# Kernel optimization log

Hardware: AMD Instinct MI355X
Metric: run time of the kernel (lower is better)

## Reference

```python
import jax, jax.numpy as jnp
import numpy as np
from jax import lax

N, T = 1024, 128
A_DIM, Z_DIM, H_DIM = 8, 32, 256


def setup_inputs() -> dict:
    key = jax.random.key(0)
    ks = jax.random.split(key, 12)
    s = 0.1  # small init scale for numerical stability of the recurrence
    return {
        "A": jax.random.normal(ks[0], (N, T, A_DIM), jnp.float32),
        "eps": jax.random.normal(ks[1], (N, T, Z_DIM), jnp.float32),
        "z0": jnp.zeros((1, Z_DIM), jnp.float32),
        "h0": jnp.zeros((1, H_DIM), jnp.float32),
        "c0": jnp.zeros((1, H_DIM), jnp.float32),
        "W_ih": jax.random.normal(ks[2], (4 * H_DIM, A_DIM + Z_DIM), jnp.float32) * s,
        "W_hh": jax.random.normal(ks[3], (4 * H_DIM, H_DIM), jnp.float32) * s,
        "b_ih": jax.random.normal(ks[4], (4 * H_DIM,), jnp.float32) * s,
        "b_hh": jax.random.normal(ks[5], (4 * H_DIM,), jnp.float32) * s,
        "W1": jax.random.normal(ks[6], (128, H_DIM), jnp.float32) * s,
        "b1": jax.random.normal(ks[7], (128,), jnp.float32) * s,
        "W2": jax.random.normal(ks[8], (128, 128), jnp.float32) * s,
        "b2": jax.random.normal(ks[9], (128,), jnp.float32) * s,
        "Wz": jax.random.normal(ks[10], (2 * Z_DIM, 128), jnp.float32) * s,
        "bz": jax.random.normal(ks[11], (2 * Z_DIM,), jnp.float32) * s,
    }


def reference(A, eps, z0, h0, c0, W_ih, W_hh, b_ih, b_hh, W1, b1, W2, b2, Wz, bz):
    """BayesianSequenceModel.guide: per-step LSTMCell + encoder MLP +
    reparameterized Gaussian draw z_t = loc + softplus(raw_scale) * eps_t.
    Returns Z with shape [N, T, z_size]."""
    n = A.shape[0]
    zdim = eps.shape[-1]

    def step(carry, xs):
        z, h, c = carry
        a_t, e_t = xs
        x = jnp.concatenate([a_t, z], axis=-1)                    # [N, a+z]
        gates = x @ W_ih.T + b_ih + h @ W_hh.T + b_hh             # [N, 4H]
        i, f, g, o = jnp.split(gates, 4, axis=-1)                 # torch LSTMCell order
        c_new = jax.nn.sigmoid(f) * c + jax.nn.sigmoid(i) * jnp.tanh(g)
        h_new = jax.nn.sigmoid(o) * jnp.tanh(c_new)
        # Encoder
        u = jax.nn.relu(h_new @ W1.T + b1)
        u = jax.nn.relu(u @ W2.T + b2)
        zz = u @ Wz.T + bz                                        # [N, 2*zdim]
        z_loc = zz[:, :zdim]
        z_scale = jax.nn.softplus(zz[:, zdim:])
        z_new = z_loc + z_scale * e_t                             # reparameterized sample
        return (z_new, h_new, c_new), z_new

    carry0 = (
        jnp.broadcast_to(z0, (n, z0.shape[1])),
        jnp.broadcast_to(h0, (n, h0.shape[1])),
        jnp.broadcast_to(c0, (n, c0.shape[1])),
    )
    xs = (jnp.swapaxes(A, 0, 1), jnp.swapaxes(eps, 0, 1))         # time-major
    _, Zs = lax.scan(step, carry0, xs)                            # [T, N, zdim]
    return jnp.swapaxes(Zs, 0, 1)                                 # [N, T, zdim]
```

## Files before the change

### kernel.cpp

```cpp
#include <hip/hip_runtime.h>
#include <hip/hip_bf16.h>
#include <math.h>

typedef __bf16 bf16x8 __attribute__((ext_vector_type(8)));
typedef float floatx4 __attribute__((ext_vector_type(4)));

#define T_LEN 128

#define WP_OFF   0
#define WP_SZ    (64*10*64*16)
#define W1P_OFF  (WP_OFF + WP_SZ)
#define W1P_SZ   (8*8*64*16)
#define W2P_OFF  (W1P_OFF + W1P_SZ)
#define W2P_SZ   (8*4*64*16)
#define WZP_OFF  (W2P_OFF + W2P_SZ)
#define WZP_SZ   (4*4*64*16)
#define WS_NEEDED ((size_t)(WZP_OFF + WZP_SZ))

#define WAITVM(N) (((N) & 0xF) | (0x7 << 4) | (0xF << 8) | (((N) >> 4) << 14))

#define BAR() do {                                                  \
    asm volatile("s_waitcnt lgkmcnt(0)" ::: "memory");              \
    __builtin_amdgcn_sched_barrier(0);                              \
    __builtin_amdgcn_s_barrier();                                   \
    __builtin_amdgcn_sched_barrier(0);                              \
} while (0)

#if __has_builtin(__builtin_amdgcn_exp2f)
#define EXP2F(x) __builtin_amdgcn_exp2f(x)
#else
#define EXP2F(x) exp2f(x)
#endif
#if __has_builtin(__builtin_amdgcn_logf)
#define LOG2F(x) __builtin_amdgcn_logf(x)
#else
#define LOG2F(x) log2f(x)
#endif
#if __has_builtin(__builtin_amdgcn_rcpf)
#define RCPF(x) __builtin_amdgcn_rcpf(x)
#else
#define RCPF(x) (1.0f/(x))
#endif

__device__ __forceinline__ float fsigmoid(float x) {
    return RCPF(1.0f + EXP2F(-1.4426950408889634f * x));
}
__device__ __forceinline__ float ftanh(float x) {
    return 1.0f - 2.0f * RCPF(1.0f + EXP2F(2.8853900817779268f * x));
}

__device__ __forceinline__ void dma16(const void* g, void* lds) {
    __builtin_amdgcn_global_load_lds(
        (const __attribute__((address_space(1))) void*)g,
        (__attribute__((address_space(3))) void*)lds,
        16, 0, 0);
}

__global__ void prep_kernel(const float* __restrict__ Wih, const float* __restrict__ Whh,
                            const float* __restrict__ W1,  const float* __restrict__ W2,
                            const float* __restrict__ Wz,  unsigned char* __restrict__ ws)
{
    int id = blockIdx.x * blockDim.x + threadIdx.x;
    __bf16* Wp  = (__bf16*)(ws + WP_OFF);
    __bf16* W1p = (__bf16*)(ws + W1P_OFF);
    __bf16* W2p = (__bf16*)(ws + W2P_OFF);
    __bf16* Wzp = (__bf16*)(ws + WZP_OFF);
    if (id < 40960) {
        int ct = id / 640, rem = id % 640;
        int ki = rem / 64, lane = rem % 64;
        int row = ct * 16 + (lane & 15);
        int kb  = ki * 32 + (lane >> 4) * 8;
        for (int j = 0; j < 8; ++j) {
            int k = kb + j;
            float v;
            if (k < 40)       v = Wih[row * 40 + k];
            else if (k < 296) v = Whh[row * 256 + (k - 40)];
            else              v = 0.0f;
            Wp[((size_t)(ki * 64 + ct) * 64 + lane) * 8 + j] = (__bf16)v;
        }
    } else if (id < 45056) {
        int id2 = id - 40960;
        int rem = id2 % 512, lane = rem % 64;
        int row = (id2 / 512) * 16 + (lane & 15);
        int kb  = (rem / 64) * 32 + (lane >> 4) * 8;
        for (int j = 0; j < 8; ++j) W1p[(size_t)id2 * 8 + j] = (__bf16)W1[row * 256 + kb + j];
    } else if (id < 47104) {
        int id3 = id - 45056;
        int rem = id3 % 256, lane = rem % 64;
        int row = (id3 / 256) * 16 + (lane & 15);
        int kb  = (rem / 64) * 32 + (lane >> 4) * 8;
        for (int j = 0; j < 8; ++j) W2p[(size_t)id3 * 8 + j] = (__bf16)W2[row * 128 + kb + j];
    } else if (id < 48128) {
        int id4 = id - 47104;
        int rem = id4 % 256, lane = rem % 64;
        int row = (id4 / 256) * 16 + (lane & 15);
        int kb  = (rem / 64) * 32 + (lane >> 4) * 8;
        for (int j = 0; j < 8; ++j) Wzp[(size_t)id4 * 8 + j] = (__bf16)Wz[row * 128 + kb + j];
    }
}

__global__ __launch_bounds__(512) void seq_mfma(
    const float* __restrict__ A,   const float* __restrict__ eps,
    const float* __restrict__ z0,  const float* __restrict__ h0,
    const float* __restrict__ c0,
    const float* __restrict__ bih, const float* __restrict__ bhh,
    const float* __restrict__ b1,  const float* __restrict__ b2,
    const float* __restrict__ bz,
    const unsigned char* __restrict__ ws, float* __restrict__ out)
{
    const int tid  = threadIdx.x;
    const int w    = tid >> 6;
    const int lane = tid & 63;
    const int lrow = lane & 15;
    const int quad = lane >> 4;
    const int n0   = blockIdx.x * 16;

    __shared__ __align__(16) __bf16 slots[8][2][2048];
    __shared__ __align__(16) __bf16 wmlp2[(W2P_SZ + WZP_SZ) / 2];
    __shared__ __align__(16) __bf16 xh[2][16][328];
    __shared__ __align__(16) __bf16 u1s[16][136];
    __shared__ __align__(16) __bf16 u2s[16][136];
    float* zzf = (float*)&u1s[0][0];

    const char* wsb = (const char*)ws;

    {
        const float4* src = (const float4*)(wsb + W2P_OFF);
        float4* dst = (float4*)wmlp2;
        for (int i = tid; i < 3072; i += 512) dst[i] = src[i];
    }
    const __bf16* w2l = wmlp2;
    const __bf16* wzl = wmlp2 + 16384;

    for (int idx = tid; idx < 2 * 16 * 320; idx += 512) {
        int b = idx / (16 * 320);
        int rem = idx % (16 * 320);
        int r = rem / 320, col = rem % 320;
        float v;
        if (col >= 8 && col < 40)        v = z0[col - 8];
        else if (col >= 40 && col < 296) v = h0[col - 40];
        else                             v = 0.0f;
        xh[b][r][col] = (__bf16)v;
    }
    if (tid < 128)
        xh[0][tid >> 3][tid & 7] =
            (__bf16)A[((size_t)(n0 + (tid >> 3)) * T_LEN + 0) * 8 + (tid & 7)];

    bf16x8 w1f[8];
    #pragma unroll
    for (int k = 0; k < 8; ++k)
        w1f[k] = *(const bf16x8*)(wsb + W1P_OFF + ((size_t)(w * 8 + k) * 64 + lane) * 16);

    float gb[4][2];
    #pragma unroll
    for (int g = 0; g < 4; ++g)
        #pragma unroll
        for (int j = 0; j < 2; ++j) {
            int unit = 32 * w + 16 * j + lrow;
            gb[g][j] = bih[g * 256 + unit] + bhh[g * 256 + unit];
        }
    float u1b = b1[w * 16 + lrow];
    float u2b = b2[w * 16 + lrow];
    float zzb = (w < 4) ? bz[w * 16 + lrow] : 0.0f;
    float cst[2][4];
    #pragma unroll
    for (int j = 0; j < 2; ++j) {
        float cv = c0[32 * w + 16 * j + lrow];
        #pragma unroll
        for (int r = 0; r < 4; ++r) cst[j][r] = cv;
    }

    #define ISSUEK0(H) do {                                                     \
        _Pragma("unroll")                                                       \
        for (int gg = 0; gg < 2; ++gg)                                          \
            _Pragma("unroll")                                                   \
            for (int j = 0; j < 2; ++j)                                         \
                dma16(wsb + WP_OFF +                                            \
                      ((size_t)((2 * (H) + gg) * 16 + 2 * w + j) * 1024) +      \
                      (size_t)lane * 16,                                        \
                      (void*)&slots[w][H][(gg * 2 + j) * 512]);                 \
    } while (0)

    ISSUEK0(0);
    ISSUEK0(1);
    __syncthreads();

    #define GHALF(KI, H, NW, DOREF) do {                                        \
        __builtin_amdgcn_s_waitcnt(WAITVM(NW));                                 \
        __builtin_amdgcn_sched_barrier(0);                                      \
        _Pragma("unroll")                                                       \
        for (int gg = 0; gg < 2; ++gg)                                          \
            _Pragma("unroll")                                                   \
            for (int j = 0; j < 2; ++j) {                                       \
                bf16x8 b_ = *(const bf16x8*)&slots[w][H][(gg * 2 + j) * 512 +   \
                                                         lane * 8];             \
                acc[2 * (H) + gg][j] = __builtin_amdgcn_mfma_f32_16x16x32_bf16( \
                    af, b_, acc[2 * (H) + gg][j], 0, 0, 0);                     \
            }                                                                   \
        __builtin_amdgcn_sched_barrier(0);                                      \
        if (DOREF) {                                                            \
            _Pragma("unroll")                                                   \
            for (int gg = 0; gg < 2; ++gg)                                      \
                _Pragma("unroll")                                               \
                for (int j = 0; j < 2; ++j)                                     \
                    dma16(wsb + WP_OFF + (size_t)((KI) + 1) * 65536 +           \
                          ((size_t)((2 * (H) + gg) * 16 + 2 * w + j) * 1024) +  \
                          (size_t)lane * 16,                                    \
                          (void*)&slots[w][H][(gg * 2 + j) * 512]);             \
        }                                                                       \
    } while (0)

    #define GKI(KI, NA, NB, DOREF) do {                                         \
        bf16x8 af = *(const bf16x8*)&xh[cb][lrow][(KI) * 32 + quad * 8];        \
        GHALF(KI, 0, NA, DOREF);                                                \
        GHALF(KI, 1, NB, DOREF);                                                \
    } while (0)

    for (int t = 0; t < T_LEN; ++t) {
        const int cb = t & 1;
        const int nb = cb ^ 1;

        float eps_cur = eps[((size_t)(n0 + (tid >> 5)) * T_LEN + t) * 32 + (tid & 31)];
        float a_nxt = 0.0f;
        if (t + 1 < T_LEN && tid < 128)
            a_nxt = A[((size_t)(n0 + (tid >> 3)) * T_LEN + (t + 1)) * 8 + (tid & 7)];

        floatx4 acc[4][2];
        #pragma unroll
        for (int g = 0; g < 4; ++g)
            #pragma unroll
            for (int j = 0; j < 2; ++j)
                acc[g][j] = (floatx4){gb[g][j], gb[g][j], gb[g][j], gb[g][j]};

        GKI(0, 7, 7, 1);
        GKI(1, 4, 4, 1);
        GKI(2, 4, 4, 1);
        GKI(3, 4, 4, 1);
        GKI(4, 4, 4, 1);
        GKI(5, 4, 4, 1);
        GKI(6, 4, 4, 1);
        GKI(7, 4, 4, 1);
        GKI(8, 4, 4, 1);
        GKI(9, 4, 0, 0);

        #pragma unroll
        for (int j = 0; j < 2; ++j)
            #pragma unroll
            for (int r = 0; r < 4; ++r) {
                float iv = fsigmoid(acc[0][j][r]);
                float fv = fsigmoid(acc[1][j][r]);
                float gv = ftanh(acc[2][j][r]);
                float ov = fsigmoid(acc[3][j][r]);
                float cn = fv * cst[j][r] + iv * gv;
                cst[j][r] = cn;
                xh[nb][quad * 4 + r][40 + 32 * w + 16 * j + lrow] = (__bf16)(ov * ftanh(cn));
            }
        if (t + 1 < T_LEN && tid < 128)
            xh[nb][tid >> 3][tid & 7] = (__bf16)a_nxt;
        BAR();

        {
            floatx4 a1 = (floatx4){u1b, u1b, u1b, u1b};
            #pragma unroll
            for (int ki = 0; ki < 8; ++ki) {
                bf16x8 af = *(const bf16x8*)&xh[nb][lrow][40 + ki * 32 + quad * 8];
                a1 = __builtin_amdgcn_mfma_f32_16x16x32_bf16(af, w1f[ki], a1, 0, 0, 0);
            }
            #pragma unroll
            for (int r = 0; r < 4; ++r)
                u1s[quad * 4 + r][w * 16 + lrow] = (__bf16)fmaxf(a1[r], 0.0f);
        }
        BAR();

        {
            floatx4 a2 = (floatx4){u2b, u2b, u2b, u2b};
            #pragma unroll
            for (int ki = 0; ki < 4; ++ki) {
                bf16x8 af = *(const bf16x8*)&u1s[lrow][ki * 32 + quad * 8];
                bf16x8 bb = *(const bf16x8*)&w2l[w * 2048 + ki * 512 + lane * 8];
                a2 = __builtin_amdgcn_mfma_f32_16x16x32_bf16(af, bb, a2, 0, 0, 0);
            }
            #pragma unroll
            for (int r = 0; r < 4; ++r)
                u2s[quad * 4 + r][w * 16 + lrow] = (__bf16)fmaxf(a2[r], 0.0f);
        }
        ISSUEK0(0);
        BAR();

        if (w < 4) {
            floatx4 a3 = (floatx4){zzb, zzb, zzb, zzb};
            #pragma unroll
            for (int ki = 0; ki < 4; ++ki) {
                bf16x8 af = *(const bf16x8*)&u2s[lrow][ki * 32 + quad * 8];
                bf16x8 bb = *(const bf16x8*)&wzl[w * 2048 + ki * 512 + lane * 8];
                a3 = __builtin_amdgcn_mfma_f32_16x16x32_bf16(af, bb, a3, 0, 0, 0);
            }
            #pragma unroll
            for (int r = 0; r < 4; ++r)
                zzf[(quad * 4 + r) * 68 + w * 16 + lrow] = a3[r];
        }
        ISSUEK0(1);
        BAR();

        {
            int r = tid >> 5, c = tid & 31;
            float loc = zzf[r * 68 + c];
            float raw = zzf[r * 68 + c + 32];
            float sp  = (raw > 20.0f)
                      ? raw
                      : 0.6931471805599453f *
                        LOG2F(1.0f + EXP2F(1.4426950408889634f * raw));
            float zv  = loc + sp * eps_cur;
            xh[nb][r][8 + c] = (__bf16)zv;
            out[((size_t)(n0 + r) * T_LEN + t) * 32 + c] = zv;
        }
        BAR();
    }
    #undef GKI
    #undef GHALF
    #undef ISSUEK0
}

struct SM {
    float zx[4][40]; float h[4][256]; float u1[4][128]; float u2[4][128]; float zz[4][64];
};

__global__ __launch_bounds__(256) void seq_valu(
    const float* __restrict__ A, const float* __restrict__ eps,
    const float* __restrict__ z0, const float* __restrict__ h0, const float* __restrict__ c0,
    const float* __restrict__ Wih, const float* __restrict__ Whh,
    const float* __restrict__ bih, const float* __restrict__ bhh,
    const float* __restrict__ W1, const float* __restrict__ b1,
    const float* __restrict__ W2, const float* __restrict__ b2,
    const float* __restrict__ Wz, const float* __restrict__ bz, float* __restrict__ out)
{
    __shared__ SM sm;
    const int tid = threadIdx.x;
    const int n0  = blockIdx.x * 4;
    if (tid < 128) { int rr = tid >> 5, cc = tid & 31; sm.zx[rr][8 + cc] = z0[cc]; }
    for (int i = tid; i < 4 * 256; i += 256) sm.h[i >> 8][i & 255] = h0[i & 255];
    float c[4];
    #pragma unroll
    for (int rr = 0; rr < 4; ++rr) c[rr] = c0[tid];
    float gbias[4];
    #pragma unroll
    for (int g = 0; g < 4; ++g) gbias[g] = bih[g * 256 + tid] + bhh[g * 256 + tid];

    for (int t = 0; t < T_LEN; ++t) {
        if (tid < 32) { int rr = tid >> 3, cc = tid & 7;
            sm.zx[rr][cc] = A[((size_t)(n0 + rr) * T_LEN + t) * 8 + cc]; }
        __syncthreads();
        float acc[4][4];
        #pragma unroll
        for (int g = 0; g < 4; ++g)
            #pragma unroll
            for (int rr = 0; rr < 4; ++rr) acc[g][rr] = gbias[g];
        for (int k = 0; k < 40; ++k) {
            float xv[4];
            #pragma unroll
            for (int rr = 0; rr < 4; ++rr) xv[rr] = sm.zx[rr][k];
            #pragma unroll
            for (int g = 0; g < 4; ++g) {
                float w = Wih[(size_t)(g * 256 + tid) * 40 + k];
                #pragma unroll
                for (int rr = 0; rr < 4; ++rr) acc[g][rr] += w * xv[rr];
            }
        }
        for (int k = 0; k < 256; ++k) {
            float hv[4];
            #pragma unroll
            for (int rr = 0; rr < 4; ++rr) hv[rr] = sm.h[rr][k];
            #pragma unroll
            for (int g = 0; g < 4; ++g) {
                float w = Whh[(size_t)(g * 256 + tid) * 256 + k];
                #pragma unroll
                for (int rr = 0; rr < 4; ++rr) acc[g][rr] += w * hv[rr];
            }
        }
        __syncthreads();
        #pragma unroll
        for (int rr = 0; rr < 4; ++rr) {
            float iv = 1.0f / (1.0f + expf(-acc[0][rr]));
            float fv = 1.0f / (1.0f + expf(-acc[1][rr]));
            float gv = tanhf(acc[2][rr]);
            float ov = 1.0f / (1.0f + expf(-acc[3][rr]));
            float cn = fv * c[rr] + iv * gv;
            c[rr] = cn;
            sm.h[rr][tid] = ov * tanhf(cn);
        }
        __syncthreads();
        { int col = tid & 127, rb = (tid >> 7) * 2;
          float a0 = b1[col], a1 = a0;
          for (int k = 0; k < 256; ++k) { float w = W1[(size_t)col * 256 + k];
              a0 += w * sm.h[rb][k]; a1 += w * sm.h[rb + 1][k]; }
          sm.u1[rb][col] = fmaxf(a0, 0.0f); sm.u1[rb + 1][col] = fmaxf(a1, 0.0f); }
        __syncthreads();
        { int col = tid & 127, rb = (tid >> 7) * 2;
          float a0 = b2[col], a1 = a0;
          for (int k = 0; k < 128; ++k) { float w = W2[(size_t)col * 128 + k];
              a0 += w * sm.u1[rb][k]; a1 += w * sm.u1[rb + 1][k]; }
          sm.u2[rb][col] = fmaxf(a0, 0.0f); sm.u2[rb + 1][col] = fmaxf(a1, 0.0f); }
        __syncthreads();
        { int rr = tid >> 6, col = tid & 63;
// ... 49 lines not shown
```

Before: 1.340 ms.

## Software-pipeline encoder MLP into next step's LSTM gate GEMM

Reorders the packed K dimension so h comes first, then z, then a. The encoder's first layer (h @ W1) can then be computed alongside the h-part of the next step's gate GEMM, and the z-dependent and a-dependent K chunks are deferred until after the encoder output is ready. The z output projection and softplus sampling are fused into two waves writing directly to xh and out, which removes the zz staging buffer and one barrier. The last timestep's encoder is peeled into an epilogue. The intent is to shorten the per-step serial critical path, at the cost of more complex weight-streaming order and wait counts.

```diff
diff --git a/kernel.cpp b/kernel.cpp
--- a/kernel.cpp
+++ b/kernel.cpp
@@ -73,8 +73,9 @@
         for (int j = 0; j < 8; ++j) {
             int k = kb + j;
             float v;
-            if (k < 40)       v = Wih[row * 40 + k];
-            else if (k < 296) v = Whh[row * 256 + (k - 40)];
+            if (k < 256)      v = Whh[row * 256 + k];
+            else if (k < 288) v = Wih[row * 40 + 8 + (k - 256)];
+            else if (k < 296) v = Wih[row * 40 + (k - 288)];
             else              v = 0.0f;
             Wp[((size_t)(ki * 64 + ct) * 64 + lane) * 8 + j] = (__bf16)v;
         }
@@ -120,7 +121,6 @@
     __shared__ __align__(16) __bf16 xh[2][16][328];
     __shared__ __align__(16) __bf16 u1s[16][136];
     __shared__ __align__(16) __bf16 u2s[16][136];
-    float* zzf = (float*)&u1s[0][0];
 
     const char* wsb = (const char*)ws;
 
@@ -137,13 +137,13 @@
         int rem = idx % (16 * 320);
         int r = rem / 320, col = rem % 320;
         float v;
-        if (col >= 8 && col < 40)        v = z0[col - 8];
-        else if (col >= 40 && col < 296) v = h0[col - 40];
-        else                             v = 0.0f;
+        if (col < 256)      v = h0[col];
+        else if (col < 288) v = z0[col - 256];
+        else                v = 0.0f;
         xh[b][r][col] = (__bf16)v;
     }
     if (tid < 128)
-        xh[0][tid >> 3][tid & 7] =
+        xh[0][tid >> 3][288 + (tid & 7)] =
             (__bf16)A[((size_t)(n0 + (tid >> 3)) * T_LEN + 0) * 8 + (tid & 7)];
 
     bf16x8 w1f[8];
@@ -161,7 +161,8 @@
         }
     float u1b = b1[w * 16 + lrow];
     float u2b = b2[w * 16 + lrow];
-    float zzb = (w < 4) ? bz[w * 16 + lrow] : 0.0f;
+    float bzl = bz[(w & 1) * 16 + lrow];
+    float bzr = bz[32 + (w & 1) * 16 + lrow];
     float cst[2][4];
     #pragma unroll
     for (int j = 0; j < 2; ++j) {
@@ -170,79 +171,128 @@
         for (int r = 0; r < 4; ++r) cst[j][r] = cv;
     }
 
-    #define ISSUEK0(H) do {                                                     \
+    #define WAITN(N) do { __builtin_amdgcn_s_waitcnt(WAITVM(N)); \
+        __builtin_amdgcn_sched_barrier(0); } while (0)
+    #define RFILL(RKI, H) do {                                                  \
         _Pragma("unroll")                                                       \
         for (int gg = 0; gg < 2; ++gg)                                          \
             _Pragma("unroll")                                                   \
             for (int j = 0; j < 2; ++j)                                         \
-                dma16(wsb + WP_OFF +                                            \
+                dma16(wsb + WP_OFF + (size_t)(RKI) * 65536 +                    \
                       ((size_t)((2 * (H) + gg) * 16 + 2 * w + j) * 1024) +      \
                       (size_t)lane * 16,                                        \
                       (void*)&slots[w][H][(gg * 2 + j) * 512]);                 \
     } while (0)
-
-    ISSUEK0(0);
-    ISSUEK0(1);
-    __syncthreads();
-
-    #define GHALF(KI, H, NW, DOREF) do {                                        \
-        __builtin_amdgcn_s_waitcnt(WAITVM(NW));                                 \
-        __builtin_amdgcn_sched_barrier(0);                                      \
+    #define CHALF(H) do {                                                       \
         _Pragma("unroll")                                                       \
         for (int gg = 0; gg < 2; ++gg)                                          \
             _Pragma("unroll")                                                   \
             for (int j = 0; j < 2; ++j) {                                       \
-                bf16x8 b_ = *(const bf16x8*)&slots[w][H][(gg * 2 + j) * 512 +   \
-                                                         lane * 8];             \
+                bf16x8 b_ = *(const bf16x8*)&slots[w][H][(gg * 2 + j) * 512     \
+                                                         + lane * 8];           \
                 acc[2 * (H) + gg][j] = __builtin_amdgcn_mfma_f32_16x16x32_bf16( \
                     af, b_, acc[2 * (H) + gg][j], 0, 0, 0);                     \
             }                                                                   \
         __builtin_amdgcn_sched_barrier(0);                                      \
-        if (DOREF) {                                                            \
-            _Pragma("unroll")                                                   \
-            for (int gg = 0; gg < 2; ++gg)                                      \
-                _Pragma("unroll")                                               \
-                for (int j = 0; j < 2; ++j)                                     \
-                    dma16(wsb + WP_OFF + (size_t)((KI) + 1) * 65536 +           \
-                          ((size_t)((2 * (H) + gg) * 16 + 2 * w + j) * 1024) +  \
-                          (size_t)lane * 16,                                    \
-                          (void*)&slots[w][H][(gg * 2 + j) * 512]);             \
-        }                                                                       \
     } while (0)
-
-    #define GKI(KI, NA, NB, DOREF) do {                                         \
+    #define GATEKI(KI, RKI, WA, WB) do {                                        \
         bf16x8 af = *(const bf16x8*)&xh[cb][lrow][(KI) * 32 + quad * 8];        \
-        GHALF(KI, 0, NA, DOREF);                                                \
-        GHALF(KI, 1, NB, DOREF);                                                \
+        WAITN(WA); CHALF(0); RFILL(RKI, 0);                                     \
+        WAITN(WB); CHALF(1); RFILL(RKI, 1);                                     \
     } while (0)
+    #define GATEKI_U1(KI, RKI, WA, WB) do {                                     \
+        bf16x8 af = *(const bf16x8*)&xh[cb][lrow][(KI) * 32 + quad * 8];        \
+        WAITN(WA); CHALF(0); RFILL(RKI, 0);                                     \
+        WAITN(WB); CHALF(1); RFILL(RKI, 1);                                     \
+        a1 = __builtin_amdgcn_mfma_f32_16x16x32_bf16(af, w1f[KI], a1, 0, 0, 0); \
+    } while (0)
+
+    RFILL(0, 0);
+    RFILL(0, 1);
+    __syncthreads();
+
+    float epsr[4];
+    float av = 0.0f;
+    const int aidx = (w & 1) * 64 + lane;
 
     for (int t = 0; t < T_LEN; ++t) {
         const int cb = t & 1;
         const int nb = cb ^ 1;
 
-        float eps_cur = eps[((size_t)(n0 + (tid >> 5)) * T_LEN + t) * 32 + (tid & 31)];
-        float a_nxt = 0.0f;
-        if (t + 1 < T_LEN && tid < 128)
-            a_nxt = A[((size_t)(n0 + (tid >> 3)) * T_LEN + (t + 1)) * 8 + (tid & 7)];
-
         floatx4 acc[4][2];
         #pragma unroll
         for (int g = 0; g < 4; ++g)
             #pragma unroll
             for (int j = 0; j < 2; ++j)
                 acc[g][j] = (floatx4){gb[g][j], gb[g][j], gb[g][j], gb[g][j]};
-
-        GKI(0, 7, 7, 1);
-        GKI(1, 4, 4, 1);
-        GKI(2, 4, 4, 1);
-        GKI(3, 4, 4, 1);
-        GKI(4, 4, 4, 1);
-        GKI(5, 4, 4, 1);
-        GKI(6, 4, 4, 1);
-        GKI(7, 4, 4, 1);
-        GKI(8, 4, 4, 1);
-        GKI(9, 4, 0, 0);
-
+        floatx4 a1 = (floatx4){u1b, u1b, u1b, u1b};
+
+        GATEKI_U1(0, 1, 4, 4);
+        __builtin_amdgcn_sched_barrier(0);
+        {
+            const int te = (t > 0) ? (t - 1) : 0;
+            #pragma unroll
+            for (int r = 0; r < 4; ++r)
+                epsr[r] = eps[((size_t)(n0 + quad * 4 + r) * T_LEN + te) * 32
+                              + (w & 1) * 16 + lrow];
+            const int ta = (t + 1 < T_LEN) ? (t + 1) : (T_LEN - 1);
+            av = A[((size_t)(n0 + (aidx >> 3)) * T_LEN + ta) * 8 + (aidx & 7)];
+        }
+        __builtin_amdgcn_sched_barrier(0);
+        GATEKI_U1(1, 2, 9, 9);
+        GATEKI_U1(2, 3, 4, 4);
+        GATEKI_U1(3, 4, 4, 4);
+        GATEKI_U1(4, 5, 4, 4);
+        GATEKI_U1(5, 6, 4, 4);
+        GATEKI_U1(6, 7, 4, 4);
+        GATEKI_U1(7, 9, 4, 4);
+        #pragma unroll
+        for (int r = 0; r < 4; ++r)
+            u1s[quad * 4 + r][w * 16 + lrow] = (__bf16)fmaxf(a1[r], 0.0f);
+        BAR();
+
+        GATEKI(9, 8, 4, 4);
+        {
+            floatx4 a2 = (floatx4){u2b, u2b, u2b, u2b};
+            #pragma unroll
+            for (int ki = 0; ki < 4; ++ki) {
+                bf16x8 af = *(const bf16x8*)&u1s[lrow][ki * 32 + quad * 8];
+                bf16x8 bb = *(const bf16x8*)&w2l[w * 2048 + ki * 512 + lane * 8];
+                a2 = __builtin_amdgcn_mfma_f32_16x16x32_bf16(af, bb, a2, 0, 0, 0);
+            }
+            #pragma unroll
+            for (int r = 0; r < 4; ++r)
+                u2s[quad * 4 + r][w * 16 + lrow] = (__bf16)fmaxf(a2[r], 0.0f);
+        }
+        BAR();
+
+        if (w < 2 && t > 0) {
+            floatx4 aL = (floatx4){bzl, bzl, bzl, bzl};
+            floatx4 aR = (floatx4){bzr, bzr, bzr, bzr};
+            #pragma unroll
+            for (int ki = 0; ki < 4; ++ki) {
+                bf16x8 af = *(const bf16x8*)&u2s[lrow][ki * 32 + quad * 8];
+                bf16x8 bl = *(const bf16x8*)&wzl[(w)     * 2048 + ki * 512 + lane * 8];
+                bf16x8 br = *(const bf16x8*)&wzl[(w + 2) * 2048 + ki * 512 + lane * 8];
+                aL = __builtin_amdgcn_mfma_f32_16x16x32_bf16(af, bl, aL, 0, 0, 0);
+                aR = __builtin_amdgcn_mfma_f32_16x16x32_bf16(af, br, aR, 0, 0, 0);
+            }
+            #pragma unroll
+            for (int r = 0; r < 4; ++r) {
+                float raw = aR[r];
+                float sp  = (raw > 20.0f)
+                          ? raw
+                          : 0.6931471805599453f *
+                            LOG2F(1.0f + EXP2F(1.4426950408889634f * raw));
+                float zv  = aL[r] + sp * epsr[r];
+                xh[cb][quad * 4 + r][256 + w * 16 + lrow] = (__bf16)zv;
+                out[((size_t)(n0 + quad * 4 + r) * T_LEN + (t - 1)) * 32
+                    + w * 16 + lrow] = zv;
+            }
+        }
+        BAR();
+
+        GATEKI(8, 0, 4, 4);
         #pragma unroll
         for (int j = 0; j < 2; ++j)
             #pragma unroll
@@ -253,72 +303,70 @@
                 float ov = fsigmoid(acc[3][j][r]);
                 float cn = fv * cst[j][r] + iv * gv;
                 cst[j][r] = cn;
-                xh[nb][quad * 4 + r][40 + 32 * w + 16 * j + lrow] = (__bf16)(ov * ftanh(cn));
-            }
-        if (t + 1 < T_LEN && tid < 128)
-            xh[nb][tid >> 3][tid & 7] = (__bf16)a_nxt;
+                xh[nb][quad * 4 + r][32 * w + 16 * j + lrow] = (__bf16)(ov * ftanh(cn));
+            }
+        if (w < 2 && t + 1 < T_LEN)
+            xh[nb][aidx >> 3][288 + (aidx & 7)] = (__bf16)av;
         BAR();
-
-        {
-            floatx4 a1 = (floatx4){u1b, u1b, u1b, u1b};
-            #pragma unroll
-            for (int ki = 0; ki < 8; ++ki) {
-                bf16x8 af = *(const bf16x8*)&xh[nb][lrow][40 + ki * 32 + quad * 8];
-                a1 = __builtin_amdgcn_mfma_f32_16x16x32_bf16(af, w1f[ki], a1, 0, 0, 0);
-            }
-            #pragma unroll
-            for (int r = 0; r < 4; ++r)
-                u1s[quad * 4 + r][w * 16 + lrow] = (__bf16)fmaxf(a1[r], 0.0f);
-        }
+    }
+
+    asm volatile("s_waitcnt vmcnt(0)" ::: "memory");
+    __builtin_amdgcn_sched_barrier(0);
+    {
+        #pragma unroll
+        for (int r = 0; r < 4; ++r)
+            epsr[r] = eps[((size_t)(n0 + quad * 4 + r) * T_LEN + (T_LEN - 1)) * 32
+                          + (w & 1) * 16 + lrow];
+        floatx4 a1 = (floatx4){u1b, u1b, u1b, u1b};
+        #pragma unroll
+        for (int ki = 0; ki < 8; ++ki) {
+            bf16x8 af = *(const bf16x8*)&xh[0][lrow][ki * 32 + quad * 8];
+            a1 = __builtin_amdgcn_mfma_f32_16x16x32_bf16(af, w1f[ki], a1, 0, 0, 0);
+        }
+        #pragma unroll
+        for (int r = 0; r < 4; ++r)
+            u1s[quad * 4 + r][w * 16 + lrow] = (__bf16)fmaxf(a1[r], 0.0f);
         BAR();
-
-        {
-            floatx4 a2 = (floatx4){u2b, u2b, u2b, u2b};
-            #pragma unroll
-            for (int ki = 0; ki < 4; ++ki) {
-                bf16x8 af = *(const bf16x8*)&u1s[lrow][ki * 32 + quad * 8];
-                bf16x8 bb = *(const bf16x8*)&w2l[w * 2048 + ki * 512 + lane * 8];
-                a2 = __builtin_amdgcn_mfma_f32_16x16x32_bf16(af, bb, a2, 0, 0, 0);
-            }
-            #pragma unroll
-            for (int r = 0; r < 4; ++r)
-                u2s[quad * 4 + r][w * 16 + lrow] = (__bf16)fmaxf(a2[r], 0.0f);
-        }
-        ISSUEK0(0);
+        floatx4 a2 = (floatx4){u2b, u2b, u2b, u2b};
+        #pragma unroll
+        for (int ki = 0; ki < 4; ++ki) {
+            bf16x8 af = *(const bf16x8*)&u1s[lrow][ki * 32 + quad * 8];
+            bf16x8 bb = *(const bf16x8*)&w2l[w * 2048 + ki * 512 + lane * 8];
+            a2 = __builtin_amdgcn_mfma_f32_16x16x32_bf16(af, bb, a2, 0, 0, 0);
+        }
+        #pragma unroll
+        for (int r = 0; r < 4; ++r)
+            u2s[quad * 4 + r][w * 16 + lrow] = (__bf16)fmaxf(a2[r], 0.0f);
         BAR();
-
-        if (w < 4) {
-            floatx4 a3 = (floatx4){zzb, zzb, zzb, zzb};
+        if (w < 2) {
+            floatx4 aL = (floatx4){bzl, bzl, bzl, bzl};
+            floatx4 aR = (floatx4){bzr, bzr, bzr, bzr};
             #pragma unroll
             for (int ki = 0; ki < 4; ++ki) {
                 bf16x8 af = *(const bf16x8*)&u2s[lrow][ki * 32 + quad * 8];
-                bf16x8 bb = *(const bf16x8*)&wzl[w * 2048 + ki * 512 + lane * 8];
-                a3 = __builtin_amdgcn_mfma_f32_16x16x32_bf16(af, bb, a3, 0, 0, 0);
-            }
-            #pragma unroll
-            for (int r = 0; r < 4; ++r)
-                zzf[(quad * 4 + r) * 68 + w * 16 + lrow] = a3[r];
-        }
-        ISSUEK0(1);
-        BAR();
-
-        {
-            int r = tid >> 5, c = tid & 31;
-            float loc = zzf[r * 68 + c];
-            float raw = zzf[r * 68 + c + 32];
-            float sp  = (raw > 20.0f)
-                      ? raw
-                      : 0.6931471805599453f *
-                        LOG2F(1.0f + EXP2F(1.4426950408889634f * raw));
-            float zv  = loc + sp * eps_cur;
-            xh[nb][r][8 + c] = (__bf16)zv;
-            out[((size_t)(n0 + r) * T_LEN + t) * 32 + c] = zv;
-        }
-        BAR();
-    }
-    #undef GKI
-    #undef GHALF
-    #undef ISSUEK0
+                bf16x8 bl = *(const bf16x8*)&wzl[(w)     * 2048 + ki * 512 + lane * 8];
+                bf16x8 br = *(const bf16x8*)&wzl[(w + 2) * 2048 + ki * 512 + lane * 8];
+                aL = __builtin_amdgcn_mfma_f32_16x16x32_bf16(af, bl, aL, 0, 0, 0);
+                aR = __builtin_amdgcn_mfma_f32_16x16x32_bf16(af, br, aR, 0, 0, 0);
+            }
+            #pragma unroll
+            for (int r = 0; r < 4; ++r) {
+                float raw = aR[r];
+                float sp  = (raw > 20.0f)
+                          ? raw
+                          : 0.6931471805599453f *
+                            LOG2F(1.0f + EXP2F(1.4426950408889634f * raw));
+                float zv  = aL[r] + sp * epsr[r];
+                out[((size_t)(n0 + quad * 4 + r) * T_LEN + (T_LEN - 1)) * 32
+                    + w * 16 + lrow] = zv;
+            }
+        }
+    }
+    #undef GATEKI_U1
+    #undef GATEKI
+    #undef CHALF
+    #undef RFILL
+    #undef WAITN
 }
 
 struct SM {
```

Result: slower. 1.599 ms (+19.3%).

## Deepen weight-streaming pipeline to four slots and stream MLP weights through it

Applied to the files above, without the earlier changes.

Replaces the two-slot per-wave gate weight ring with a four-slot ring, prefetching two k-chunks ahead so DMA has more time to land before each MFMA consumes it. The W2 and Wz MLP weights are no longer held resident in LDS; they are streamed through the same ring each step, which frees LDS. The time loop is unrolled by two so slot indices become compile-time constants, and the eps/A loads for the next step are issued early. The cost is extra global/L2 traffic for the MLP weights every step and more vmcnt bookkeeping that must stay exactly right.

```diff
diff --git a/kernel.cpp b/kernel.cpp
--- a/kernel.cpp
+++ b/kernel.cpp
@@ -115,22 +115,13 @@
     const int quad = lane >> 4;
     const int n0   = blockIdx.x * 16;
 
-    __shared__ __align__(16) __bf16 slots[8][2][2048];
-    __shared__ __align__(16) __bf16 wmlp2[(W2P_SZ + WZP_SZ) / 2];
+    __shared__ __align__(16) __bf16 slots[8][4][2048];
     __shared__ __align__(16) __bf16 xh[2][16][328];
     __shared__ __align__(16) __bf16 u1s[16][136];
     __shared__ __align__(16) __bf16 u2s[16][136];
     float* zzf = (float*)&u1s[0][0];
 
     const char* wsb = (const char*)ws;
-
-    {
-        const float4* src = (const float4*)(wsb + W2P_OFF);
-        float4* dst = (float4*)wmlp2;
-        for (int i = tid; i < 3072; i += 512) dst[i] = src[i];
-    }
-    const __bf16* w2l = wmlp2;
-    const __bf16* wzl = wmlp2 + 16384;
 
     for (int idx = tid; idx < 2 * 16 * 320; idx += 512) {
         int b = idx / (16 * 320);
@@ -170,155 +161,198 @@
         for (int r = 0; r < 4; ++r) cst[j][r] = cv;
     }
 
-    #define ISSUEK0(H) do {                                                     \
+    #define DMAG(KI, H, SL) do {                                                \
         _Pragma("unroll")                                                       \
         for (int gg = 0; gg < 2; ++gg)                                          \
             _Pragma("unroll")                                                   \
             for (int j = 0; j < 2; ++j)                                         \
-                dma16(wsb + WP_OFF +                                            \
+                dma16(wsb + WP_OFF + (size_t)(KI) * 65536 +                     \
                       ((size_t)((2 * (H) + gg) * 16 + 2 * w + j) * 1024) +      \
                       (size_t)lane * 16,                                        \
-                      (void*)&slots[w][H][(gg * 2 + j) * 512]);                 \
+                      (void*)&slots[w][SL][(gg * 2 + j) * 512]);                \
     } while (0)
-
-    ISSUEK0(0);
-    ISSUEK0(1);
-    __syncthreads();
-
-    #define GHALF(KI, H, NW, DOREF) do {                                        \
-        __builtin_amdgcn_s_waitcnt(WAITVM(NW));                                 \
+    #define DMAW2(SL) do {                                                      \
+        _Pragma("unroll")                                                       \
+        for (int i = 0; i < 4; ++i)                                             \
+            dma16(wsb + W2P_OFF + (size_t)w * 4096 + i * 1024 +                 \
+                  (size_t)lane * 16, (void*)&slots[w][SL][i * 512]);            \
+    } while (0)
+    #define DMAWZ(SL) do {                                                      \
+        _Pragma("unroll")                                                       \
+        for (int i = 0; i < 4; ++i)                                             \
+            dma16(wsb + WZP_OFF + (size_t)(w & 3) * 4096 + i * 1024 +           \
+                  (size_t)lane * 16, (void*)&slots[w][SL][i * 512]);            \
+    } while (0)
+    #define CONSG(H, SL, WN) do {                                               \
+        __builtin_amdgcn_s_waitcnt(WAITVM(WN));                                 \
         __builtin_amdgcn_sched_barrier(0);                                      \
         _Pragma("unroll")                                                       \
         for (int gg = 0; gg < 2; ++gg)                                          \
             _Pragma("unroll")                                                   \
             for (int j = 0; j < 2; ++j) {                                       \
-                bf16x8 b_ = *(const bf16x8*)&slots[w][H][(gg * 2 + j) * 512 +   \
-                                                         lane * 8];             \
+                bf16x8 b_ = *(const bf16x8*)&slots[w][SL][(gg * 2 + j) * 512    \
+                                                          + lane * 8];          \
                 acc[2 * (H) + gg][j] = __builtin_amdgcn_mfma_f32_16x16x32_bf16( \
                     af, b_, acc[2 * (H) + gg][j], 0, 0, 0);                     \
             }                                                                   \
         __builtin_amdgcn_sched_barrier(0);                                      \
-        if (DOREF) {                                                            \
-            _Pragma("unroll")                                                   \
-            for (int gg = 0; gg < 2; ++gg)                                      \
+    } while (0)
+
+    const int aidx = (w & 1) * 64 + lane;
+    float eps_cur, eps_nxt, av;
+
+    DMAG(0, 0, 0);
+    DMAG(0, 1, 1);
+    DMAG(1, 0, 2);
+    DMAG(1, 1, 3);
+    eps_cur = eps[((size_t)(n0 + (tid >> 5)) * T_LEN + 0) * 32 + (tid & 31)];
+    av      = A[((size_t)(n0 + (aidx >> 3)) * T_LEN + 1) * 8 + (aidx & 7)];
+    __syncthreads();
+
+    #define STEPBODY(OFF, T) do {                                               \
+        const int cb = (T) & 1;                                                 \
+        const int nb = cb ^ 1;                                                  \
+        floatx4 acc[4][2];                                                      \
+        _Pragma("unroll")                                                       \
+        for (int g = 0; g < 4; ++g)                                             \
+            _Pragma("unroll")                                                   \
+            for (int j = 0; j < 2; ++j)                                         \
+                acc[g][j] = (floatx4){gb[g][j], gb[g][j], gb[g][j], gb[g][j]};  \
+        {               \
+            bf16x8 af;                                                          \
+            af = *(const bf16x8*)&xh[cb][lrow][0 * 32 + quad * 8];              \
+            CONSG(0, (0  + (OFF)) & 3, 14);  DMAG(2, 0, (0  + (OFF)) & 3);      \
+            CONSG(1, (1  + (OFF)) & 3, 14);  DMAG(2, 1, (1  + (OFF)) & 3);      \
+            af = *(const bf16x8*)&xh[cb][lrow][1 * 32 + quad * 8];              \
+            CONSG(0, (2  + (OFF)) & 3, 14);  DMAG(3, 0, (2  + (OFF)) & 3);      \
+            CONSG(1, (3  + (OFF)) & 3, 14);  DMAG(3, 1, (3  + (OFF)) & 3);      \
+            af = *(const bf16x8*)&xh[cb][lrow][2 * 32 + quad * 8];              \
+            CONSG(0, (4  + (OFF)) & 3, 12);  DMAG(4, 0, (4  + (OFF)) & 3);      \
+            CONSG(1, (5  + (OFF)) & 3, 12);  DMAG(4, 1, (5  + (OFF)) & 3);      \
+            af = *(const bf16x8*)&xh[cb][lrow][3 * 32 + quad * 8];              \
+            CONSG(0, (6  + (OFF)) & 3, 12);  DMAG(5, 0, (6  + (OFF)) & 3);      \
+            CONSG(1, (7  + (OFF)) & 3, 12);  DMAG(5, 1, (7  + (OFF)) & 3);      \
+            af = *(const bf16x8*)&xh[cb][lrow][4 * 32 + quad * 8];              \
+            CONSG(0, (8  + (OFF)) & 3, 12);  DMAG(6, 0, (8  + (OFF)) & 3);      \
+            CONSG(1, (9  + (OFF)) & 3, 12);  DMAG(6, 1, (9  + (OFF)) & 3);      \
+            af = *(const bf16x8*)&xh[cb][lrow][5 * 32 + quad * 8];              \
+            CONSG(0, (10 + (OFF)) & 3, 12);  DMAG(7, 0, (10 + (OFF)) & 3);      \
+            CONSG(1, (11 + (OFF)) & 3, 12);  DMAG(7, 1, (11 + (OFF)) & 3);      \
+            af = *(const bf16x8*)&xh[cb][lrow][6 * 32 + quad * 8];              \
+            CONSG(0, (12 + (OFF)) & 3, 12);  DMAG(8, 0, (12 + (OFF)) & 3);      \
+            CONSG(1, (13 + (OFF)) & 3, 12);  DMAG(8, 1, (13 + (OFF)) & 3);      \
+            af = *(const bf16x8*)&xh[cb][lrow][7 * 32 + quad * 8];              \
+            CONSG(0, (14 + (OFF)) & 3, 12);  DMAG(9, 0, (14 + (OFF)) & 3);      \
+            CONSG(1, (15 + (OFF)) & 3, 12);  DMAG(9, 1, (15 + (OFF)) & 3);      \
+            af = *(const bf16x8*)&xh[cb][lrow][8 * 32 + quad * 8];              \
+            CONSG(0, (16 + (OFF)) & 3, 12);  DMAW2((16 + (OFF)) & 3);           \
+            CONSG(1, (17 + (OFF)) & 3, 12);  DMAWZ((17 + (OFF)) & 3);           \
+            af = *(const bf16x8*)&xh[cb][lrow][9 * 32 + quad * 8];              \
+            CONSG(0, (18 + (OFF)) & 3, 12);  DMAG(0, 0, (18 + (OFF)) & 3);      \
+            CONSG(1, (19 + (OFF)) & 3, 12);  DMAG(0, 1, (19 + (OFF)) & 3);      \
+        }                                                                       \
+                       \
+        _Pragma("unroll")                                                       \
+        for (int j = 0; j < 2; ++j)                                             \
+            _Pragma("unroll")                                                   \
+            for (int r = 0; r < 4; ++r) {                                       \
+                float iv = fsigmoid(acc[0][j][r]);                              \
+                float fv = fsigmoid(acc[1][j][r]);                              \
+                float gv = ftanh(acc[2][j][r]);                                 \
+                float ov = fsigmoid(acc[3][j][r]);                              \
+                float cn = fv * cst[j][r] + iv * gv;                            \
+                cst[j][r] = cn;                                                 \
+                xh[nb][quad * 4 + r][40 + 32 * w + 16 * j + lrow] =             \
+                    (__bf16)(ov * ftanh(cn));                                   \
+            }                                                                   \
+        if (w < 2 && (T) + 1 < T_LEN)                                           \
+            xh[nb][aidx >> 3][aidx & 7] = (__bf16)av;                           \
+        BAR();                                    \
+        {                       \
+            floatx4 a1 = (floatx4){u1b, u1b, u1b, u1b};                         \
+            _Pragma("unroll")                                                   \
+            for (int ki = 0; ki < 8; ++ki) {                                    \
+                bf16x8 af1 = *(const bf16x8*)&xh[nb][lrow][40 + ki * 32         \
+                                                           + quad * 8];        \
+                a1 = __builtin_amdgcn_mfma_f32_16x16x32_bf16(af1, w1f[ki],      \
+                                                             a1, 0, 0, 0);      \
+            }                                                                   \
+            _Pragma("unroll")                                                   \
+            for (int r = 0; r < 4; ++r)                                         \
+                u1s[quad * 4 + r][w * 16 + lrow] = (__bf16)fmaxf(a1[r], 0.0f);  \
+        }                                                                       \
+        BAR();                                               \
+        {                 \
+            __builtin_amdgcn_s_waitcnt(WAITVM(12));                             \
+            __builtin_amdgcn_sched_barrier(0);                                  \
+            floatx4 a2 = (floatx4){u2b, u2b, u2b, u2b};                         \
+            _Pragma("unroll")                                                   \
+            for (int ki = 0; ki < 4; ++ki) {                                    \
+                bf16x8 af2 = *(const bf16x8*)&u1s[lrow][ki * 32 + quad * 8];    \
+                bf16x8 bb  = *(const bf16x8*)&slots[w][(20 + (OFF)) & 3]        \
+                                                      [ki * 512 + lane * 8];    \
+                a2 = __builtin_amdgcn_mfma_f32_16x16x32_bf16(af2, bb,           \
+                                                             a2, 0, 0, 0);      \
+            }                                                                   \
+            _Pragma("unroll")                                                   \
+            for (int r = 0; r < 4; ++r)                                         \
+                u2s[quad * 4 + r][w * 16 + lrow] = (__bf16)fmaxf(a2[r], 0.0f);  \
+            __builtin_amdgcn_sched_barrier(0);                                  \
+            DMAG(1, 0, (20 + (OFF)) & 3);                                       \
+        }                                                                       \
+        BAR();                     \
+        {        \
+            __builtin_amdgcn_s_waitcnt(WAITVM(12));                             \
+            __builtin_amdgcn_sched_barrier(0);                                  \
+            if (w < 4) {                                                        \
+                floatx4 a3 = (floatx4){zzb, zzb, zzb, zzb};                     \
                 _Pragma("unroll")                                               \
-                for (int j = 0; j < 2; ++j)                                     \
-                    dma16(wsb + WP_OFF + (size_t)((KI) + 1) * 65536 +           \
-                          ((size_t)((2 * (H) + gg) * 16 + 2 * w + j) * 1024) +  \
-                          (size_t)lane * 16,                                    \
-                          (void*)&slots[w][H][(gg * 2 + j) * 512]);             \
+                for (int ki = 0; ki < 4; ++ki) {                                \
+                    bf16x8 af3 = *(const bf16x8*)&u2s[lrow][ki * 32             \
+                                                            + quad * 8];       \
+                    bf16x8 bb  = *(const bf16x8*)&slots[w][(21 + (OFF)) & 3]    \
+                                                          [ki * 512 + lane * 8];\
+                    a3 = __builtin_amdgcn_mfma_f32_16x16x32_bf16(af3, bb,       \
+                                                                 a3, 0, 0, 0);  \
+                }                                                               \
+                _Pragma("unroll")                                               \
+                for (int r = 0; r < 4; ++r)                                     \
+                    zzf[(quad * 4 + r) * 68 + w * 16 + lrow] = a3[r];           \
+            }                                                                   \
+            __builtin_amdgcn_sched_barrier(0);                                  \
+            DMAG(1, 1, (21 + (OFF)) & 3);                                       \
+            const int te = ((T) + 1 < T_LEN) ? (T) + 1 : T_LEN - 1;             \
+            eps_nxt = eps[((size_t)(n0 + (tid >> 5)) * T_LEN + te) * 32         \
+                          + (tid & 31)];                                        \
+            const int ta = ((T) + 2 < T_LEN) ? (T) + 2 : T_LEN - 1;             \
+            av = A[((size_t)(n0 + (aidx >> 3)) * T_LEN + ta) * 8 + (aidx & 7)]; \
         }                                                                       \
+        BAR();                                                \
+        {                    \
+            int r = tid >> 5, c = tid & 31;                                     \
+            float loc = zzf[r * 68 + c];                                        \
+            float raw = zzf[r * 68 + c + 32];                                   \
+            float sp  = (raw > 20.0f)                                           \
+                      ? raw                                                     \
+                      : 0.6931471805599453f *                                   \
+                        LOG2F(1.0f + EXP2F(1.4426950408889634f * raw));         \
+            float zv  = loc + sp * eps_cur;                                     \
+            xh[nb][r][8 + c] = (__bf16)zv;                                      \
+            out[((size_t)(n0 + r) * T_LEN + (T)) * 32 + c] = zv;                \
+        }                                                                       \
+        eps_cur = eps_nxt;                                                      \
+        BAR();                           \
     } while (0)
 
-    #define GKI(KI, NA, NB, DOREF) do {                                         \
-        bf16x8 af = *(const bf16x8*)&xh[cb][lrow][(KI) * 32 + quad * 8];        \
-        GHALF(KI, 0, NA, DOREF);                                                \
-        GHALF(KI, 1, NB, DOREF);                                                \
-    } while (0)
-
-    for (int t = 0; t < T_LEN; ++t) {
-        const int cb = t & 1;
-        const int nb = cb ^ 1;
-
-        float eps_cur = eps[((size_t)(n0 + (tid >> 5)) * T_LEN + t) * 32 + (tid & 31)];
-        float a_nxt = 0.0f;
-        if (t + 1 < T_LEN && tid < 128)
-            a_nxt = A[((size_t)(n0 + (tid >> 3)) * T_LEN + (t + 1)) * 8 + (tid & 7)];
-
-        floatx4 acc[4][2];
-        #pragma unroll
-        for (int g = 0; g < 4; ++g)
-            #pragma unroll
-            for (int j = 0; j < 2; ++j)
-                acc[g][j] = (floatx4){gb[g][j], gb[g][j], gb[g][j], gb[g][j]};
-
-        GKI(0, 7, 7, 1);
-        GKI(1, 4, 4, 1);
-        GKI(2, 4, 4, 1);
-        GKI(3, 4, 4, 1);
-        GKI(4, 4, 4, 1);
-        GKI(5, 4, 4, 1);
-        GKI(6, 4, 4, 1);
-        GKI(7, 4, 4, 1);
-        GKI(8, 4, 4, 1);
-        GKI(9, 4, 0, 0);
-
-        #pragma unroll
-        for (int j = 0; j < 2; ++j)
-            #pragma unroll
-            for (int r = 0; r < 4; ++r) {
-                float iv = fsigmoid(acc[0][j][r]);
-                float fv = fsigmoid(acc[1][j][r]);
-                float gv = ftanh(acc[2][j][r]);
-                float ov = fsigmoid(acc[3][j][r]);
-                float cn = fv * cst[j][r] + iv * gv;
-                cst[j][r] = cn;
-                xh[nb][quad * 4 + r][40 + 32 * w + 16 * j + lrow] = (__bf16)(ov * ftanh(cn));
-            }
-        if (t + 1 < T_LEN && tid < 128)
-            xh[nb][tid >> 3][tid & 7] = (__bf16)a_nxt;
-        BAR();
-
-        {
-            floatx4 a1 = (floatx4){u1b, u1b, u1b, u1b};
-            #pragma unroll
-            for (int ki = 0; ki < 8; ++ki) {
-                bf16x8 af = *(const bf16x8*)&xh[nb][lrow][40 + ki * 32 + quad * 8];
-                a1 = __builtin_amdgcn_mfma_f32_16x16x32_bf16(af, w1f[ki], a1, 0, 0, 0);
-            }
-            #pragma unroll
-            for (int r = 0; r < 4; ++r)
-                u1s[quad * 4 + r][w * 16 + lrow] = (__bf16)fmaxf(a1[r], 0.0f);
-        }
-        BAR();
-
-        {
-            floatx4 a2 = (floatx4){u2b, u2b, u2b, u2b};
-            #pragma unroll
-            for (int ki = 0; ki < 4; ++ki) {
-                bf16x8 af = *(const bf16x8*)&u1s[lrow][ki * 32 + quad * 8];
-                bf16x8 bb = *(const bf16x8*)&w2l[w * 2048 + ki * 512 + lane * 8];
-                a2 = __builtin_amdgcn_mfma_f32_16x16x32_bf16(af, bb, a2, 0, 0, 0);
-            }
-            #pragma unroll
-            for (int r = 0; r < 4; ++r)
-                u2s[quad * 4 + r][w * 16 + lrow] = (__bf16)fmaxf(a2[r], 0.0f);
-        }
-        ISSUEK0(0);
-        BAR();
-
-        if (w < 4) {
-            floatx4 a3 = (floatx4){zzb, zzb, zzb, zzb};
-            #pragma unroll
-            for (int ki = 0; ki < 4; ++ki) {
-                bf16x8 af = *(const bf16x8*)&u2s[lrow][ki * 32 + quad * 8];
-                bf16x8 bb = *(const bf16x8*)&wzl[w * 2048 + ki * 512 + lane * 8];
-                a3 = __builtin_amdgcn_mfma_f32_16x16x32_bf16(af, bb, a3, 0, 0, 0);
-            }
-            #pragma unroll
-            for (int r = 0; r < 4; ++r)
-                zzf[(quad * 4 + r) * 68 + w * 16 + lrow] = a3[r];
-        }
-        ISSUEK0(1);
-        BAR();
-
-        {
-            int r = tid >> 5, c = tid & 31;
-            float loc = zzf[r * 68 + c];
-            float raw = zzf[r * 68 + c + 32];
-            float sp  = (raw > 20.0f)
-                      ? raw
-                      : 0.6931471805599453f *
-                        LOG2F(1.0f + EXP2F(1.4426950408889634f * raw));
-            float zv  = loc + sp * eps_cur;
-            xh[nb][r][8 + c] = (__bf16)zv;
-            out[((size_t)(n0 + r) * T_LEN + t) * 32 + c] = zv;
-        }
-        BAR();
-    }
-    #undef GKI
-    #undef GHALF
-    #undef ISSUEK0
+    for (int t2 = 0; t2 < T_LEN; t2 += 2) {
+        STEPBODY(0, t2);
+        STEPBODY(2, t2 + 1);
+    }
+    #undef STEPBODY
+    #undef CONSG
+    #undef DMAWZ
+    #undef DMAW2
+    #undef DMAG
 }
 
 struct SM {
```

Result: slower. 1.589 ms (+18.6%).

## Double-buffer full-K weight slices and stream MLP weights through DMA ring

Applied to the files above, without the earlier changes.

Replaces the per-gate-half slot refill scheme with a two-slot ring, where each slot holds all four gates for one K-slice. The next-but-one slice is prefetched while the current one is consumed. The separately resident W2/Wz shared-memory copy is removed. Those weights now stream through the same slot ring at the end of the gate loop, which frees LDS and lets deeper prefetch run across the MLP stages. The cost is more global traffic per step (MLP weights reloaded every timestep) and carefully tuned vmcnt wait counts that must match the issue order.

```diff
diff --git a/kernel.cpp b/kernel.cpp
--- a/kernel.cpp
+++ b/kernel.cpp
@@ -25,6 +25,9 @@
     __builtin_amdgcn_s_barrier();                                   \
     __builtin_amdgcn_sched_barrier(0);                              \
 } while (0)
+
+#define WAITN(N) do { __builtin_amdgcn_s_waitcnt(WAITVM(N)); \
+    __builtin_amdgcn_sched_barrier(0); } while (0)
 
 #if __has_builtin(__builtin_amdgcn_exp2f)
 #define EXP2F(x) __builtin_amdgcn_exp2f(x)
@@ -115,22 +118,13 @@
     const int quad = lane >> 4;
     const int n0   = blockIdx.x * 16;
 
-    __shared__ __align__(16) __bf16 slots[8][2][2048];
-    __shared__ __align__(16) __bf16 wmlp2[(W2P_SZ + WZP_SZ) / 2];
+    __shared__ __align__(16) __bf16 slots[8][2][4096];
     __shared__ __align__(16) __bf16 xh[2][16][328];
     __shared__ __align__(16) __bf16 u1s[16][136];
     __shared__ __align__(16) __bf16 u2s[16][136];
     float* zzf = (float*)&u1s[0][0];
 
     const char* wsb = (const char*)ws;
-
-    {
-        const float4* src = (const float4*)(wsb + W2P_OFF);
-        float4* dst = (float4*)wmlp2;
-        for (int i = tid; i < 3072; i += 512) dst[i] = src[i];
-    }
-    const __bf16* w2l = wmlp2;
-    const __bf16* wzl = wmlp2 + 16384;
 
     for (int idx = tid; idx < 2 * 16 * 320; idx += 512) {
         int b = idx / (16 * 320);
@@ -170,55 +164,54 @@
         for (int r = 0; r < 4; ++r) cst[j][r] = cv;
     }
 
-    #define ISSUEK0(H) do {                                                     \
-        _Pragma("unroll")                                                       \
-        for (int gg = 0; gg < 2; ++gg)                                          \
-            _Pragma("unroll")                                                   \
-            for (int j = 0; j < 2; ++j)                                         \
-                dma16(wsb + WP_OFF +                                            \
-                      ((size_t)((2 * (H) + gg) * 16 + 2 * w + j) * 1024) +      \
-                      (size_t)lane * 16,                                        \
-                      (void*)&slots[w][H][(gg * 2 + j) * 512]);                 \
+    #define DMAKI(KI, SP) do {                                                \
+        _Pragma("unroll")                                                     \
+        for (int G = 0; G < 4; ++G)                                           \
+            _Pragma("unroll")                                                 \
+            for (int j = 0; j < 2; ++j)                                       \
+                dma16(wsb + WP_OFF + (size_t)(KI) * 65536 +                   \
+                      ((size_t)(G * 16 + 2 * w + j) * 1024) +                 \
+                      (size_t)lane * 16,                                      \
+                      (void*)((SP) + (G * 2 + j) * 512));                     \
     } while (0)
-
-    ISSUEK0(0);
-    ISSUEK0(1);
+    #define DMAMX(SP) do {                                                    \
+        _Pragma("unroll")                                                     \
+        for (int i = 0; i < 4; ++i)                                           \
+            dma16(wsb + W2P_OFF + (size_t)w * 4096 + (size_t)i * 1024 +       \
+                  (size_t)lane * 16, (void*)((SP) + i * 512));                \
+        _Pragma("unroll")                                                     \
+        for (int i = 0; i < 4; ++i)                                           \
+            dma16(wsb + WZP_OFF + (size_t)(w & 3) * 4096 + (size_t)i * 1024 + \
+                  (size_t)lane * 16, (void*)((SP) + (4 + i) * 512));          \
+    } while (0)
+    #define CONSKI(KI, SP, WN) do {                                           \
+        bf16x8 af = *(const bf16x8*)&xh[cb][lrow][(KI) * 32 + quad * 8];      \
+        WAITN(WN);                                                            \
+        _Pragma("unroll")                                                     \
+        for (int G = 0; G < 4; ++G)                                           \
+            _Pragma("unroll")                                                 \
+            for (int j = 0; j < 2; ++j) {                                     \
+                bf16x8 b_ = *(const bf16x8*)((SP) + (G * 2 + j) * 512         \
+                                             + lane * 8);                     \
+                acc[G][j] = __builtin_amdgcn_mfma_f32_16x16x32_bf16(          \
+                    af, b_, acc[G][j], 0, 0, 0);                              \
+            }                                                                 \
+        __builtin_amdgcn_sched_barrier(0);                                    \
+    } while (0)
+
+    __bf16* const sbase = &slots[w][0][0];
+    int sb = 0;
+
+    DMAKI(0, sbase);
+    DMAKI(1, sbase + 4096);
     __syncthreads();
-
-    #define GHALF(KI, H, NW, DOREF) do {                                        \
-        __builtin_amdgcn_s_waitcnt(WAITVM(NW));                                 \
-        __builtin_amdgcn_sched_barrier(0);                                      \
-        _Pragma("unroll")                                                       \
-        for (int gg = 0; gg < 2; ++gg)                                          \
-            _Pragma("unroll")                                                   \
-            for (int j = 0; j < 2; ++j) {                                       \
-                bf16x8 b_ = *(const bf16x8*)&slots[w][H][(gg * 2 + j) * 512 +   \
-                                                         lane * 8];             \
-                acc[2 * (H) + gg][j] = __builtin_amdgcn_mfma_f32_16x16x32_bf16( \
-                    af, b_, acc[2 * (H) + gg][j], 0, 0, 0);                     \
-            }                                                                   \
-        __builtin_amdgcn_sched_barrier(0);                                      \
-        if (DOREF) {                                                            \
-            _Pragma("unroll")                                                   \
-            for (int gg = 0; gg < 2; ++gg)                                      \
-                _Pragma("unroll")                                               \
-                for (int j = 0; j < 2; ++j)                                     \
-                    dma16(wsb + WP_OFF + (size_t)((KI) + 1) * 65536 +           \
-                          ((size_t)((2 * (H) + gg) * 16 + 2 * w + j) * 1024) +  \
-                          (size_t)lane * 16,                                    \
-                          (void*)&slots[w][H][(gg * 2 + j) * 512]);             \
-        }                                                                       \
-    } while (0)
-
-    #define GKI(KI, NA, NB, DOREF) do {                                         \
-        bf16x8 af = *(const bf16x8*)&xh[cb][lrow][(KI) * 32 + quad * 8];        \
-        GHALF(KI, 0, NA, DOREF);                                                \
-        GHALF(KI, 1, NB, DOREF);                                                \
-    } while (0)
 
     for (int t = 0; t < T_LEN; ++t) {
         const int cb = t & 1;
         const int nb = cb ^ 1;
+
+        __bf16* const s0 = sbase + sb * 4096;
+        __bf16* const s1 = sbase + (sb ^ 1) * 4096;
 
         float eps_cur = eps[((size_t)(n0 + (tid >> 5)) * T_LEN + t) * 32 + (tid & 31)];
         float a_nxt = 0.0f;
@@ -232,16 +225,16 @@
             for (int j = 0; j < 2; ++j)
                 acc[g][j] = (floatx4){gb[g][j], gb[g][j], gb[g][j], gb[g][j]};
 
-        GKI(0, 7, 7, 1);
-        GKI(1, 4, 4, 1);
-        GKI(2, 4, 4, 1);
-        GKI(3, 4, 4, 1);
-        GKI(4, 4, 4, 1);
-        GKI(5, 4, 4, 1);
-        GKI(6, 4, 4, 1);
-        GKI(7, 4, 4, 1);
-        GKI(8, 4, 4, 1);
-        GKI(9, 4, 0, 0);
+        CONSKI(0, s0, 9);   DMAKI(2, s0);
+        CONSKI(1, s1, 9);   DMAKI(3, s1);
+        CONSKI(2, s0, 8);   DMAKI(4, s0);
+        CONSKI(3, s1, 8);   DMAKI(5, s1);
+        CONSKI(4, s0, 8);   DMAKI(6, s0);
+        CONSKI(5, s1, 8);   DMAKI(7, s1);
+        CONSKI(6, s0, 8);   DMAKI(8, s0);
+        CONSKI(7, s1, 8);   DMAKI(9, s1);
+        CONSKI(8, s0, 8);   DMAMX(s0);
+        CONSKI(9, s1, 8);   DMAKI(0, s1);
 
         #pragma unroll
         for (int j = 0; j < 2; ++j)
@@ -263,8 +256,8 @@
             floatx4 a1 = (floatx4){u1b, u1b, u1b, u1b};
             #pragma unroll
             for (int ki = 0; ki < 8; ++ki) {
-                bf16x8 af = *(const bf16x8*)&xh[nb][lrow][40 + ki * 32 + quad * 8];
-                a1 = __builtin_amdgcn_mfma_f32_16x16x32_bf16(af, w1f[ki], a1, 0, 0, 0);
+                bf16x8 af1 = *(const bf16x8*)&xh[nb][lrow][40 + ki * 32 + quad * 8];
+                a1 = __builtin_amdgcn_mfma_f32_16x16x32_bf16(af1, w1f[ki], a1, 0, 0, 0);
             }
             #pragma unroll
             for (int r = 0; r < 4; ++r)
@@ -273,33 +266,35 @@
         BAR();
 
         {
+            WAITN(12);
             floatx4 a2 = (floatx4){u2b, u2b, u2b, u2b};
             #pragma unroll
             for (int ki = 0; ki < 4; ++ki) {
-                bf16x8 af = *(const bf16x8*)&u1s[lrow][ki * 32 + quad * 8];
-                bf16x8 bb = *(const bf16x8*)&w2l[w * 2048 + ki * 512 + lane * 8];
-                a2 = __builtin_amdgcn_mfma_f32_16x16x32_bf16(af, bb, a2, 0, 0, 0);
+                bf16x8 af2 = *(const bf16x8*)&u1s[lrow][ki * 32 + quad * 8];
+                bf16x8 bb  = *(const bf16x8*)(s0 + ki * 512 + lane * 8);
+                a2 = __builtin_amdgcn_mfma_f32_16x16x32_bf16(af2, bb, a2, 0, 0, 0);
             }
             #pragma unroll
             for (int r = 0; r < 4; ++r)
                 u2s[quad * 4 + r][w * 16 + lrow] = (__bf16)fmaxf(a2[r], 0.0f);
         }
-        ISSUEK0(0);
         BAR();
 
+        WAITN(8);
         if (w < 4) {
             floatx4 a3 = (floatx4){zzb, zzb, zzb, zzb};
             #pragma unroll
             for (int ki = 0; ki < 4; ++ki) {
-                bf16x8 af = *(const bf16x8*)&u2s[lrow][ki * 32 + quad * 8];
-                bf16x8 bb = *(const bf16x8*)&wzl[w * 2048 + ki * 512 + lane * 8];
-                a3 = __builtin_amdgcn_mfma_f32_16x16x32_bf16(af, bb, a3, 0, 0, 0);
+                bf16x8 af3 = *(const bf16x8*)&u2s[lrow][ki * 32 + quad * 8];
+                bf16x8 bb  = *(const bf16x8*)(s0 + (4 + ki) * 512 + lane * 8);
+                a3 = __builtin_amdgcn_mfma_f32_16x16x32_bf16(af3, bb, a3, 0, 0, 0);
             }
             #pragma unroll
             for (int r = 0; r < 4; ++r)
                 zzf[(quad * 4 + r) * 68 + w * 16 + lrow] = a3[r];
         }
-        ISSUEK0(1);
+        __builtin_amdgcn_sched_barrier(0);
+        DMAKI(1, s0);
         BAR();
 
         {
@@ -315,10 +310,11 @@
             out[((size_t)(n0 + r) * T_LEN + t) * 32 + c] = zv;
         }
         BAR();
-    }
-    #undef GKI
-    #undef GHALF
-    #undef ISSUEK0
+        sb ^= 1;
+    }
+    #undef CONSKI
+    #undef DMAMX
+    #undef DMAKI
 }
 
 struct SM {
```

Result: slower. 1.526 ms (+13.9%).
